# Kernel tuning notes

Hardware: AMD Instinct MI355X
Metric: run time of the kernel (lower is better)

The kernel has to match this reference:

```python
import jax, jax.numpy as jnp
import numpy as np

B, DIN, H = 16384, 512, 512
K = 7  # LC_i1, LC_i2, LC_f1, LC_f2, LC_o, LC_z (gate nets, idx 0..5), LC_d (decay net, idx 6)


def setup_inputs() -> dict:
    key = jax.random.key(0)
    ks = jax.random.split(key, 8)
    s1 = 1.0 / np.sqrt(DIN)
    s2 = 1.0 / np.sqrt(H)
    return {
        "hx": jax.random.normal(ks[0], (B, DIN), jnp.float32),
        "cx1": jax.random.normal(ks[1], (B, H), jnp.float32),
        "cx2": jax.random.normal(ks[2], (B, H), jnp.float32),
        # stacked params for the 7 sub-networks (same structure: Linear(DIN,H) -> Linear(H,H))
        "W1": jax.random.uniform(ks[3], (K, H, DIN), jnp.float32, -s1, s1),
        "b1": jax.random.uniform(ks[4], (K, H), jnp.float32, -s1, s1),
        "W2": jax.random.uniform(ks[5], (K, H, H), jnp.float32, -s2, s2),
        "b2": jax.random.uniform(ks[6], (K, H), jnp.float32, -s2, s2),
    }


def reference(hx, cx1, cx2, W1, b1, W2, b2):
    # layer 1 for all 7 nets at once: [K, B, H]
    h1 = jnp.einsum('bd,khd->kbh', hx, W1) + b1[:, None, :]
    # gate nets use tanh, decay net uses softplus
    a1 = jnp.concatenate([jnp.tanh(h1[:6]), jax.nn.softplus(h1[6:])], axis=0)
    # layer 2: [K, B, H]
    h2 = jnp.einsum('kbh,kgh->kbg', a1, W2) + b2[:, None, :]
    gates = jax.nn.sigmoid(jnp.tanh(h2[:6]))  # Gate_network: sigmoid(tanh(.))
    d = jax.nn.softplus(h2[6])                # Decay_network output (decay_coef, side state)
    i1, i2, f1, f2, o, zg = gates
    z = jnp.tanh(zg)                          # z = Tanh(LC_z(hx))
    cy1 = f1 * cx1 + i1 * z                   # side state self.cy1
    cy2 = f2 * cx2 + i2 * z
    return cy2
```

## Files before the change

### kernel.cpp

```cpp
#include <hip/hip_runtime.h>
#include <hip/hip_bf16.h>

typedef __attribute__((ext_vector_type(8))) __bf16 bf16x8;
typedef __attribute__((ext_vector_type(4))) __bf16 bf16x4;
typedef __attribute__((ext_vector_type(4))) float f32x4;

constexpr int M = 16384;
constexpr int K = 512;
constexpr int BK = 32;
constexpr int NT = 16;

__device__ __forceinline__ void async_copy16(const void* gsrc, void* ldst) {
  __builtin_amdgcn_global_load_lds(
      (const __attribute__((address_space(1))) unsigned int*)(gsrc),
      (__attribute__((address_space(3))) unsigned int*)(ldst),
      16, 0, 0);
}

__device__ __forceinline__ float frcp(float x) { return __builtin_amdgcn_rcpf(x); }
__device__ __forceinline__ float ftanh(float x) {
  return 1.0f - 2.0f * frcp(1.0f + __expf(2.0f * x));
}
__device__ __forceinline__ float fsigm(float x) { return frcp(1.0f + __expf(-x)); }

__device__ __forceinline__ int kswz(int row) {
  return ((row & 3) << 3) ^ ((row & 12) << 2);
}

template <int MODE>
__global__ __launch_bounds__(256) void gemm_kernel(
    const __bf16* __restrict__ Ab,
    const __bf16* __restrict__ W,
    const float* __restrict__ bias,
    __bf16* __restrict__ outb,
    const __bf16* __restrict__ gates,
    const float* __restrict__ cx2,
    float* __restrict__ outf)
{
  const int j = blockIdx.z;
  const int jj = (MODE == 3) ? 2 : j;
  const int mbase = blockIdx.x * 128;
  const int nbase = blockIdx.y * 128;
  constexpr size_t NH = (size_t)M * 512;

  const __bf16* Aj = (MODE == 1) ? Ab : Ab + (size_t)jj * NH;
  const __bf16* Wj = W + (size_t)jj * 262144;
  const int brow = 2 * jj + 1;

  __shared__ __align__(16) __bf16 smem[24576];

  const int tid  = threadIdx.x;
  const int wid  = tid >> 6;
  const int lane = tid & 63;
  const int wm   = (wid >> 1) * 64;
  const int wn   = (wid & 1) * 64;
  const int srow = wid * 16 + (lane >> 2);
  const int scol = ((lane & 3) ^ ((lane >> 3) & 3)) * 8;
  const int fr   = lane & 15;
  const int kc   = lane >> 4;
  const int sw   = (fr >> 1) & 3;
  const int rowq = kc * 4;

  auto stage = [&](int p, int k0) {
    __bf16* As = smem + p * 8192;
    __bf16* Bs = As + 4096;
#pragma unroll
    for (int r = 0; r < 2; ++r) {
      async_copy16(Aj + (size_t)(mbase + r * 64 + srow) * K + (k0 + scol),
                   (void*)&As[(r * 64 + wid * 16) * BK]);
      async_copy16(Wj + (size_t)(nbase + r * 64 + srow) * K + (k0 + scol),
                   (void*)&Bs[(r * 64 + wid * 16) * BK]);
    }
  };

  f32x4 acc[4][4] = {};

  stage(0, 0);
  stage(1, BK);
  int pr = 0, ps = 2;
  for (int t = 0; t < NT; ++t) {
    if (t < NT - 2) asm volatile("s_waitcnt vmcnt(4) lgkmcnt(0)" ::: "memory");
    else            asm volatile("s_waitcnt vmcnt(0) lgkmcnt(0)" ::: "memory");
    __builtin_amdgcn_s_barrier();
    __builtin_amdgcn_sched_barrier(0);
    if (t < NT - 2) stage(ps, (t + 2) * BK);

    const __bf16* As = smem + pr * 8192;
    const __bf16* Bs = As + 4096;
    bf16x8 af[4], bfr[4];
#pragma unroll
    for (int i = 0; i < 4; ++i) {
      af[i]  = *(const bf16x8*)&As[(wm + i * 16 + fr) * BK + ((kc ^ sw) * 8)];
      bfr[i] = *(const bf16x8*)&Bs[(wn + i * 16 + fr) * BK + ((kc ^ sw) * 8)];
    }
#pragma unroll
    for (int mi = 0; mi < 4; ++mi)
#pragma unroll
      for (int ni = 0; ni < 4; ++ni)
        acc[mi][ni] = __builtin_amdgcn_mfma_f32_16x16x32_bf16(
            af[mi], bfr[ni], acc[mi][ni], 0, 0, 0);

    pr = (pr == 2) ? 0 : pr + 1;
    ps = (ps == 2) ? 0 : ps + 1;
  }

  float bv[4];
  const float* bj = bias + (size_t)brow * 512 + nbase + wn;
#pragma unroll
  for (int ni = 0; ni < 4; ++ni) bv[ni] = bj[ni * 16 + fr];

  __syncthreads();
#pragma unroll
  for (int mi = 0; mi < 4; ++mi)
#pragma unroll
    for (int ni = 0; ni < 4; ++ni)
#pragma unroll
      for (int r = 0; r < 4; ++r) {
        float v = acc[mi][ni][r] + bv[ni];
        float res;
        if constexpr (MODE == 1) res = ftanh(v);
        else if constexpr (MODE == 2) res = fsigm(ftanh(v));
        else res = ftanh(fsigm(ftanh(v)));
        const int row = wm + mi * 16 + rowq + r;
        const int col = wn + ni * 16 + fr;
        smem[row * 128 + (col ^ kswz(row))] = (__bf16)res;
      }
  __syncthreads();

  if constexpr (MODE <= 2) {
#pragma unroll
    for (int it = 0; it < 8; ++it) {
      const int s = it * 256 + tid;
      const int row = s >> 4, ch = s & 15;
      bf16x8 v = *(const bf16x8*)&smem[row * 128 + ((ch * 8) ^ kswz(row))];
      *(bf16x8*)&outb[(size_t)j * NH + (size_t)(mbase + row) * 512 +
                      (nbase + ch * 8)] = v;
    }
  } else {
#pragma unroll
    for (int it = 0; it < 8; ++it) {
      const int s = it * 256 + tid;
      const int row = s >> 4, ch = s & 15;
      const size_t gidx = (size_t)(mbase + row) * 512 + (nbase + ch * 8);
      bf16x8 zv = *(const bf16x8*)&smem[row * 128 + ((ch * 8) ^ kswz(row))];
      bf16x8 i2 = *(const bf16x8*)&gates[gidx];
      bf16x8 f2 = *(const bf16x8*)&gates[NH + gidx];
      f32x4 c0 = *(const f32x4*)&cx2[gidx];
      f32x4 c1 = *(const f32x4*)&cx2[gidx + 4];
      f32x4 r0, r1;
#pragma unroll
      for (int q = 0; q < 4; ++q) {
        r0[q] = (float)f2[q] * c0[q] + (float)i2[q] * (float)zv[q];
        r1[q] = (float)f2[4 + q] * c1[q] + (float)i2[4 + q] * (float)zv[4 + q];
      }
      *(f32x4*)&outf[gidx] = r0;
      *(f32x4*)&outf[gidx + 4] = r1;
    }
  }
}

__global__ __launch_bounds__(256) void cvt_all(const float* __restrict__ hx,
                                               const float* __restrict__ W1,
                                               const float* __restrict__ W2,
                                               __bf16* __restrict__ hxb,
                                               __bf16* __restrict__ Wb) {
  const int b = blockIdx.x;
  if (b < 1536) {
    const int y = b >> 8;
    const int bb = b & 255;
    const float* src = (y < 3) ? W1 + (size_t)(2 * y + 1) * 262144
                               : W2 + (size_t)(2 * (y - 3) + 1) * 262144;
    __bf16* d = Wb + (size_t)y * 262144;
    const size_t i = ((size_t)bb * 256 + threadIdx.x) * 4;
    f32x4 v = *(const f32x4*)&src[i];
    *(bf16x4*)&d[i] = __builtin_convertvector(v, bf16x4);
  } else {
    const size_t i = ((size_t)(b - 1536) * 256 + threadIdx.x) * 4;
    f32x4 v = *(const f32x4*)&hx[i];
    *(bf16x4*)&hxb[i] = __builtin_convertvector(v, bf16x4);
  }
}

extern "C" void kernel_launch(void* const* d_in, const int* in_sizes, int n_in,
                              void* d_out, int out_size, void* d_ws, size_t ws_size,
                              hipStream_t stream) {
  const float* hx  = (const float*)d_in[0];
  const float* cx2 = (const float*)d_in[2];
  const float* W1  = (const float*)d_in[3];
  const float* b1  = (const float*)d_in[4];
  const float* W2  = (const float*)d_in[5];
  const float* b2  = (const float*)d_in[6];
  float* out = (float*)d_out;

  char* ws = (char*)d_ws;
  __bf16* Wb    = (__bf16*)(ws);
  __bf16* hxb   = (__bf16*)(ws + 3145728);
  __bf16* a1    = (__bf16*)(ws + 19922944);
  __bf16* gates = (__bf16*)(ws + 70254592);
  __bf16* W2b   = Wb + 3 * 262144;

  cvt_all<<<9728, 256, 0, stream>>>(hx, W1, W2, hxb, Wb);

  gemm_kernel<1><<<dim3(128, 4, 3), 256, 0, stream>>>(
      hxb, Wb, b1, a1, nullptr, nullptr, nullptr);
  gemm_kernel<2><<<dim3(128, 4, 2), 256, 0, stream>>>(
      a1, W2b, b2, gates, nullptr, nullptr, nullptr);
  gemm_kernel<3><<<dim3(128, 4, 1), 256, 0, stream>>>(
      a1, W2b, b2, nullptr, gates, cx2, out);
}
```

Measured before the change: 224.1 us.

## Enlarge GEMM M-tile to 256, merge layer-2 launches, split elementwise epilogue

The block M-tile doubles to 256 rows, so each wave computes an 8x4 MFMA fragment grid, with larger LDS buffers and a waves_per_eu hint. The three layer-2 gate GEMMs now run in one launch, with the z gate picking its activation at runtime. The final cell update moves into a separate elementwise kernel. This cuts launches and B-operand reloads, but adds a round trip of the z gate through global memory, raises register pressure, and halves the block count per GEMM.

```diff
diff --git a/kernel.cpp b/kernel.cpp
--- a/kernel.cpp
+++ b/kernel.cpp
@@ -28,18 +28,15 @@
 }
 
 template <int MODE>
-__global__ __launch_bounds__(256) void gemm_kernel(
+__global__ __launch_bounds__(256)
+__attribute__((amdgpu_waves_per_eu(2))) void gemm_kernel(
     const __bf16* __restrict__ Ab,
     const __bf16* __restrict__ W,
     const float* __restrict__ bias,
-    __bf16* __restrict__ outb,
-    const __bf16* __restrict__ gates,
-    const float* __restrict__ cx2,
-    float* __restrict__ outf)
+    __bf16* __restrict__ outb)
 {
-  const int j = blockIdx.z;
-  const int jj = (MODE == 3) ? 2 : j;
-  const int mbase = blockIdx.x * 128;
+  const int jj = blockIdx.z;
+  const int mbase = blockIdx.x * 256;
   const int nbase = blockIdx.y * 128;
   constexpr size_t NH = (size_t)M * 512;
 
@@ -47,12 +44,12 @@
   const __bf16* Wj = W + (size_t)jj * 262144;
   const int brow = 2 * jj + 1;
 
-  __shared__ __align__(16) __bf16 smem[24576];
+  __shared__ __align__(16) __bf16 smem[36864];
 
   const int tid  = threadIdx.x;
   const int wid  = tid >> 6;
   const int lane = tid & 63;
-  const int wm   = (wid >> 1) * 64;
+  const int wm   = (wid >> 1) * 128;
   const int wn   = (wid & 1) * 64;
   const int srow = wid * 16 + (lane >> 2);
   const int scol = ((lane & 3) ^ ((lane >> 3) & 3)) * 8;
@@ -62,39 +59,41 @@
   const int rowq = kc * 4;
 
   auto stage = [&](int p, int k0) {
-    __bf16* As = smem + p * 8192;
-    __bf16* Bs = As + 4096;
-#pragma unroll
-    for (int r = 0; r < 2; ++r) {
+    __bf16* As = smem + p * 12288;
+    __bf16* Bs = As + 8192;
+#pragma unroll
+    for (int r = 0; r < 4; ++r)
       async_copy16(Aj + (size_t)(mbase + r * 64 + srow) * K + (k0 + scol),
                    (void*)&As[(r * 64 + wid * 16) * BK]);
+#pragma unroll
+    for (int r = 0; r < 2; ++r)
       async_copy16(Wj + (size_t)(nbase + r * 64 + srow) * K + (k0 + scol),
                    (void*)&Bs[(r * 64 + wid * 16) * BK]);
-    }
   };
 
-  f32x4 acc[4][4] = {};
+  f32x4 acc[8][4] = {};
 
   stage(0, 0);
   stage(1, BK);
   int pr = 0, ps = 2;
   for (int t = 0; t < NT; ++t) {
-    if (t < NT - 2) asm volatile("s_waitcnt vmcnt(4) lgkmcnt(0)" ::: "memory");
+    if (t < NT - 2) asm volatile("s_waitcnt vmcnt(6) lgkmcnt(0)" ::: "memory");
     else            asm volatile("s_waitcnt vmcnt(0) lgkmcnt(0)" ::: "memory");
     __builtin_amdgcn_s_barrier();
     __builtin_amdgcn_sched_barrier(0);
     if (t < NT - 2) stage(ps, (t + 2) * BK);
 
-    const __bf16* As = smem + pr * 8192;
-    const __bf16* Bs = As + 4096;
-    bf16x8 af[4], bfr[4];
-#pragma unroll
-    for (int i = 0; i < 4; ++i) {
+    const __bf16* As = smem + pr * 12288;
+    const __bf16* Bs = As + 8192;
+    bf16x8 af[8], bfr[4];
+#pragma unroll
+    for (int i = 0; i < 8; ++i)
       af[i]  = *(const bf16x8*)&As[(wm + i * 16 + fr) * BK + ((kc ^ sw) * 8)];
+#pragma unroll
+    for (int i = 0; i < 4; ++i)
       bfr[i] = *(const bf16x8*)&Bs[(wn + i * 16 + fr) * BK + ((kc ^ sw) * 8)];
-    }
-#pragma unroll
-    for (int mi = 0; mi < 4; ++mi)
+#pragma unroll
+    for (int mi = 0; mi < 8; ++mi)
 #pragma unroll
       for (int ni = 0; ni < 4; ++ni)
         acc[mi][ni] = __builtin_amdgcn_mfma_f32_16x16x32_bf16(
@@ -111,7 +110,7 @@
 
   __syncthreads();
 #pragma unroll
-  for (int mi = 0; mi < 4; ++mi)
+  for (int mi = 0; mi < 8; ++mi)
 #pragma unroll
     for (int ni = 0; ni < 4; ++ni)
 #pragma unroll
@@ -119,43 +118,43 @@
         float v = acc[mi][ni][r] + bv[ni];
         float res;
         if constexpr (MODE == 1) res = ftanh(v);
-        else if constexpr (MODE == 2) res = fsigm(ftanh(v));
-        else res = ftanh(fsigm(ftanh(v)));
+        else res = (jj == 2) ? ftanh(fsigm(ftanh(v)))
+                             : fsigm(ftanh(v));
         const int row = wm + mi * 16 + rowq + r;
         const int col = wn + ni * 16 + fr;
         smem[row * 128 + (col ^ kswz(row))] = (__bf16)res;
       }
   __syncthreads();
-
-  if constexpr (MODE <= 2) {
-#pragma unroll
-    for (int it = 0; it < 8; ++it) {
-      const int s = it * 256 + tid;
-      const int row = s >> 4, ch = s & 15;
-      bf16x8 v = *(const bf16x8*)&smem[row * 128 + ((ch * 8) ^ kswz(row))];
-      *(bf16x8*)&outb[(size_t)j * NH + (size_t)(mbase + row) * 512 +
-                      (nbase + ch * 8)] = v;
+#pragma unroll
+  for (int it = 0; it < 16; ++it) {
+    const int s = it * 256 + tid;
+    const int row = s >> 4, ch = s & 15;
+    bf16x8 v = *(const bf16x8*)&smem[row * 128 + ((ch * 8) ^ kswz(row))];
+    *(bf16x8*)&outb[(size_t)jj * NH + (size_t)(mbase + row) * 512 +
+                    (nbase + ch * 8)] = v;
+  }
+}
+
+__global__ __launch_bounds__(256) void final_kernel(
+    const __bf16* __restrict__ gates, const float* __restrict__ cx2,
+    float* __restrict__ out)
+{
+  constexpr size_t NH = (size_t)M * 512;
+  const size_t i = ((size_t)blockIdx.x * 256 + threadIdx.x) * 8;
+  bf16x8 i2 = *(const bf16x8*)&gates[i];
+  bf16x8 f2 = *(const bf16x8*)&gates[NH + i];
+  bf16x8 zz = *(const bf16x8*)&gates[2 * NH + i];
+  f32x4 c0 = *(const f32x4*)&cx2[i];
+  f32x4 c1 = *(const f32x4*)&cx2[i + 4];
+#pragma unroll
+  for (int h = 0; h < 2; ++h) {
+    f32x4 r;
+#pragma unroll
+    for (int q = 0; q < 4; ++q) {
+      const int e = h * 4 + q;
+      r[q] = (float)f2[e] * (h ? c1[q] : c0[q]) + (float)i2[e] * (float)zz[e];
     }
-  } else {
-#pragma unroll
-    for (int it = 0; it < 8; ++it) {
-      const int s = it * 256 + tid;
-      const int row = s >> 4, ch = s & 15;
-      const size_t gidx = (size_t)(mbase + row) * 512 + (nbase + ch * 8);
-      bf16x8 zv = *(const bf16x8*)&smem[row * 128 + ((ch * 8) ^ kswz(row))];
-      bf16x8 i2 = *(const bf16x8*)&gates[gidx];
-      bf16x8 f2 = *(const bf16x8*)&gates[NH + gidx];
-      f32x4 c0 = *(const f32x4*)&cx2[gidx];
-      f32x4 c1 = *(const f32x4*)&cx2[gidx + 4];
-      f32x4 r0, r1;
-#pragma unroll
-      for (int q = 0; q < 4; ++q) {
-        r0[q] = (float)f2[q] * c0[q] + (float)i2[q] * (float)zv[q];
-        r1[q] = (float)f2[4 + q] * c1[q] + (float)i2[4 + q] * (float)zv[4 + q];
-      }
-      *(f32x4*)&outf[gidx] = r0;
-      *(f32x4*)&outf[gidx + 4] = r1;
-    }
+    *(f32x4*)&out[i + h * 4] = r;
   }
 }
 
@@ -201,10 +200,7 @@
 
   cvt_all<<<9728, 256, 0, stream>>>(hx, W1, W2, hxb, Wb);
 
-  gemm_kernel<1><<<dim3(128, 4, 3), 256, 0, stream>>>(
-      hxb, Wb, b1, a1, nullptr, nullptr, nullptr);
-  gemm_kernel<2><<<dim3(128, 4, 2), 256, 0, stream>>>(
-      a1, W2b, b2, gates, nullptr, nullptr, nullptr);
-  gemm_kernel<3><<<dim3(128, 4, 1), 256, 0, stream>>>(
-      a1, W2b, b2, nullptr, gates, cx2, out);
-}
+  gemm_kernel<1><<<dim3(64, 4, 3), 256, 0, stream>>>(hxb, Wb, b1, a1);
+  gemm_kernel<2><<<dim3(64, 4, 3), 256, 0, stream>>>(a1, W2b, b2, gates);
+  final_kernel<<<4096, 256, 0, stream>>>(gates, cx2, out);
+}
```

Measured after the change: 233.7 us. 4.3% more time.
